# Kernel tuning notes

Measured on AMD Instinct MI355X. Metric: run time of the kernel, lower is better.

## Reference

```python
import jax, jax.numpy as jnp
import numpy as np

B, R, S, H = 4, 64, 512, 768
E = 64            # candidate entities per example
SEG = 128         # seg_emb_dim
NT, NC, NP = 6, 13, 3
REP = 3 * H + 2 * SEG  # rel_rep_size = 2560
NEG = -1e30


def setup_inputs() -> dict:
    key = jax.random.key(0)
    ks = jax.random.split(key, 12)
    hidden_states = jax.random.normal(ks[0], (B, S, H), dtype=jnp.float32)
    rel_pairs = jax.random.randint(ks[1], (B, R, 2), 0, E, dtype=jnp.int64)
    rel_masks = jax.random.randint(ks[2], (B, R, S), 0, 2, dtype=jnp.int32)
    rel_sizes = jax.random.randint(ks[3], (B, R, 2), 0, 30, dtype=jnp.int64)
    ent_span_reps = jax.random.normal(ks[4], (B, E, H), dtype=jnp.float32)
    ent_segs_embs = jax.random.normal(ks[5], (B, E, SEG), dtype=jnp.float32)
    s = 1.0 / np.sqrt(REP)
    W_type = jax.random.uniform(ks[6], (REP, NT), jnp.float32, -s, s)
    b_type = jax.random.uniform(ks[7], (NT,), jnp.float32, -s, s)
    W_cate = jax.random.uniform(ks[8], (REP, NC), jnp.float32, -s, s)
    b_cate = jax.random.uniform(ks[9], (NC,), jnp.float32, -s, s)
    W_pola = jax.random.uniform(ks[10], (REP, NP), jnp.float32, -s, s)
    b_pola = jax.random.uniform(ks[11], (NP,), jnp.float32, -s, s)
    return {"hidden_states": hidden_states, "rel_pairs": rel_pairs,
            "rel_masks": rel_masks, "rel_sizes": rel_sizes,
            "ent_span_reps": ent_span_reps, "ent_segs_embs": ent_segs_embs,
            "W_type": W_type, "b_type": b_type, "W_cate": W_cate,
            "b_cate": b_cate, "W_pola": W_pola, "b_pola": b_pola}


def reference(hidden_states, rel_pairs, rel_masks, rel_sizes,
              ent_span_reps, ent_segs_embs,
              W_type, b_type, W_cate, b_cate, W_pola, b_pola):
    batch, max_rels, _ = rel_pairs.shape
    # batched gather: ent_span_reps[b, rel_pairs[b]] -> [B, R, 2, H] -> [B, R, 2H]
    pair_span = jnp.take_along_axis(
        ent_span_reps[:, :, None, :],
        rel_pairs[:, None, :, :, None].reshape(batch, max_rels * 2, 1, 1), axis=1
    ).reshape(batch, max_rels, -1)
    pair_segs = jnp.take_along_axis(
        ent_segs_embs[:, :, None, :],
        rel_pairs[:, None, :, :, None].reshape(batch, max_rels * 2, 1, 1), axis=1
    ).reshape(batch, max_rels, -1)
    # masked max over seq: scores [B, R, S, H]
    mask_add = (rel_masks == 0).astype(jnp.float32) * NEG          # [B, R, S]
    ctx = jnp.max(hidden_states[:, None, :, :] + mask_add[..., None], axis=2)  # [B, R, H]
    has_ctx = jnp.any(rel_masks != 0, axis=-1)                      # [B, R]
    ctx = jnp.where(has_ctx[..., None], ctx, 0.0)
    features = jnp.concatenate([pair_span, pair_segs, ctx], axis=2)  # [B, R, 2560]
    # dropout is identity at inference
    rel_type_logits = features @ W_type + b_type
    rel_cate_logits = features @ W_cate + b_cate
    rel_pola_logits = features @ W_pola + b_pola
    return (rel_type_logits, rel_cate_logits, rel_pola_logits)
```

## Files before the change

### kernel.cpp

```cpp
#include <hip/hip_runtime.h>
#include <math.h>

#define BB 4
#define RR 64
#define SS 512
#define HH 768
#define EE 64
#define SEGD 128
#define NT 6
#define NC 13
#define NP 3
#define NO (NT + NC + NP)
#define REP 2560
#define NEGV -1e30f

#define HC 8
#define NHB (HH / HC)
#define SCP 4
#define SROWS (SS / SCP)
#define NB1 (BB * NHB * SCP)
#define PART_ELEMS ((size_t)BB * RR * SCP * HH)

__global__ __launch_bounds__(256, 6)
void p1_ctx(const float* __restrict__ hidden,
            const int*   __restrict__ rel_masks,
            float* __restrict__ ws)
{
    const int bid = blockIdx.x;
    const int sc  = bid & 3;
    const int hc  = (bid >> 2) % NHB;
    const int b   = bid / (4 * NHB);
    const int t   = threadIdx.x;
    const int w   = t >> 6;
    const int r   = t & 63;
    const int h0  = hc * HC;
    const int s0  = sc * SROWS;

    __shared__ unsigned char keep[64 * 132];
    __shared__ float part[4 * 64 * 9];

    const int mbase = b * RR * SS + s0;
    for (int k = t; k < 64 * SROWS; k += 256) {
        const int rr = k >> 7;
        const int s  = k & 127;
        keep[rr * 132 + s] = (unsigned char)(rel_masks[(size_t)mbase + rr * SS + s] != 0);
    }
    __syncthreads();

    float a0 = -INFINITY, a1 = -INFINITY, a2 = -INFINITY, a3 = -INFINITY;
    float a4 = -INFINITY, a5 = -INFINITY, a6 = -INFINITY, a7 = -INFINITY;
    const float* hp = hidden + ((size_t)b * SS + s0 + w * 32) * HH + h0;
    const unsigned char* kp = &keep[r * 132 + w * 32];
#pragma unroll 4
    for (int s = 0; s < 32; ++s) {
        const float4 va = *reinterpret_cast<const float4*>(hp + (size_t)s * HH);
        const float4 vb = *reinterpret_cast<const float4*>(hp + (size_t)s * HH + 4);
        const float a = kp[s] ? 0.f : NEGV;
        a0 = fmaxf(a0, va.x + a);
        a1 = fmaxf(a1, va.y + a);
        a2 = fmaxf(a2, va.z + a);
        a3 = fmaxf(a3, va.w + a);
        a4 = fmaxf(a4, vb.x + a);
        a5 = fmaxf(a5, vb.y + a);
        a6 = fmaxf(a6, vb.z + a);
        a7 = fmaxf(a7, vb.w + a);
    }

    float* pp = &part[(w * 64 + r) * 9];
    pp[0] = a0; pp[1] = a1; pp[2] = a2; pp[3] = a3;
    pp[4] = a4; pp[5] = a5; pp[6] = a6; pp[7] = a7;
    __syncthreads();

    if (w == 0) {
        float* wp = ws + (((size_t)(b * RR + r)) * SCP + sc) * HH + h0;
#pragma unroll
        for (int j = 0; j < 8; ++j) {
            float v = part[(0 * 64 + r) * 9 + j];
            v = fmaxf(v, part[(1 * 64 + r) * 9 + j]);
            v = fmaxf(v, part[(2 * 64 + r) * 9 + j]);
            v = fmaxf(v, part[(3 * 64 + r) * 9 + j]);
            wp[j] = v;
        }
    }
}

__global__ __launch_bounds__(256)
void p2_head(const float* __restrict__ ws,
             const int*   __restrict__ rel_pairs,
             const float* __restrict__ span,
             const float* __restrict__ segs,
             const float* __restrict__ Wt, const float* __restrict__ bt,
             const float* __restrict__ Wc, const float* __restrict__ bc,
             const float* __restrict__ Wp, const float* __restrict__ bp,
             float* __restrict__ out)
{
    const int br = blockIdx.x;
    const int b  = br / RR;
    const int t  = threadIdx.x;

    __shared__ float feat[REP];
    __shared__ float red[4][NO];

    const int i0 = rel_pairs[(size_t)br * 2 + 0];
    const int i1 = rel_pairs[(size_t)br * 2 + 1];

    const float* sp0 = span + ((size_t)b * EE + i0) * HH;
    const float* sp1 = span + ((size_t)b * EE + i1) * HH;
    feat[t]            = sp0[t];
    feat[t + 256]      = sp0[t + 256];
    feat[t + 512]      = sp0[t + 512];
    feat[HH + t]       = sp1[t];
    feat[HH + t + 256] = sp1[t + 256];
    feat[HH + t + 512] = sp1[t + 512];
    const float* sg0 = segs + ((size_t)b * EE + i0) * SEGD;
    const float* sg1 = segs + ((size_t)b * EE + i1) * SEGD;
    if (t < SEGD) feat[2 * HH + t] = sg0[t];
    else          feat[2 * HH + SEGD + (t - SEGD)] = sg1[t - SEGD];

    const float* wbase = ws + (size_t)br * SCP * HH;
    float m0 = -INFINITY, m1 = -INFINITY, m2 = -INFINITY;
#pragma unroll
    for (int c = 0; c < SCP; ++c) {
        const float* wp = wbase + (size_t)c * HH;
        m0 = fmaxf(m0, wp[t]);
        m1 = fmaxf(m1, wp[t + 256]);
        m2 = fmaxf(m2, wp[t + 512]);
    }
    if (m0 < -1e29f) m0 = 0.f;
    if (m1 < -1e29f) m1 = 0.f;
    if (m2 < -1e29f) m2 = 0.f;
    const int CTX0 = 2 * HH + 2 * SEGD;
    feat[CTX0 + t]       = m0;
    feat[CTX0 + t + 256] = m1;
    feat[CTX0 + t + 512] = m2;
    __syncthreads();

    float acc[NO];
#pragma unroll
    for (int o = 0; o < NO; ++o) acc[o] = 0.f;
    for (int f = t; f < REP; f += 256) {
        const float fv = feat[f];
        const float* wt = Wt + (size_t)f * NT;
        const float* wc = Wc + (size_t)f * NC;
        const float* wp = Wp + (size_t)f * NP;
#pragma unroll
        for (int o = 0; o < NT; ++o) acc[o]           += fv * wt[o];
#pragma unroll
        for (int o = 0; o < NC; ++o) acc[NT + o]      += fv * wc[o];
#pragma unroll
        for (int o = 0; o < NP; ++o) acc[NT + NC + o] += fv * wp[o];
    }
#pragma unroll
    for (int o = 0; o < NO; ++o) {
#pragma unroll
        for (int off = 32; off > 0; off >>= 1)
            acc[o] += __shfl_down(acc[o], off, 64);
    }
    const int wid  = t >> 6;
    const int lane = t & 63;
    if (lane == 0) {
#pragma unroll
        for (int o = 0; o < NO; ++o) red[wid][o] = acc[o];
    }
    __syncthreads();

    if (t < NO) {
        const float v = red[0][t] + red[1][t] + red[2][t] + red[3][t];
        if (t < NT) {
            out[(size_t)br * NT + t] = v + bt[t];
        } else if (t < NT + NC) {
            const int o = t - NT;
            out[(size_t)BB * RR * NT + (size_t)br * NC + o] = v + bc[o];
        } else {
            const int o = t - NT - NC;
            out[(size_t)BB * RR * (NT + NC) + (size_t)br * NP + o] = v + bp[o];
        }
    }
}

__global__ __launch_bounds__(256)
void rel_cls_fused(const float* __restrict__ hidden,
                   const int*   __restrict__ rel_pairs,
                   const int*   __restrict__ rel_masks,
                   const float* __restrict__ span,
                   const float* __restrict__ segs,
                   const float* __restrict__ Wt, const float* __restrict__ bt,
                   const float* __restrict__ Wc, const float* __restrict__ bc,
                   const float* __restrict__ Wp, const float* __restrict__ bp,
                   float* __restrict__ out)
{
    const int br = blockIdx.x;
    const int b  = br / RR;
    const int t  = threadIdx.x;

    __shared__ float sadd[SS];
    __shared__ float feat[REP];
    __shared__ float red[4][NO];

    const int* mrow = rel_masks + (size_t)br * SS;
    sadd[t]       = mrow[t] ? 0.f : NEGV;
    sadd[t + 256] = mrow[t + 256] ? 0.f : NEGV;

    const int i0 = rel_pairs[(size_t)br * 2 + 0];
    const int i1 = rel_pairs[(size_t)br * 2 + 1];
    const float* sp0 = span + ((size_t)b * EE + i0) * HH;
    const float* sp1 = span + ((size_t)b * EE + i1) * HH;
    feat[t]            = sp0[t];
    feat[t + 256]      = sp0[t + 256];
    feat[t + 512]      = sp0[t + 512];
    feat[HH + t]       = sp1[t];
    feat[HH + t + 256] = sp1[t + 256];
    feat[HH + t + 512] = sp1[t + 512];
    const float* sg0 = segs + ((size_t)b * EE + i0) * SEGD;
    const float* sg1 = segs + ((size_t)b * EE + i1) * SEGD;
    if (t < SEGD) feat[2 * HH + t] = sg0[t];
    else          feat[2 * HH + SEGD + (t - SEGD)] = sg1[t - SEGD];
    __syncthreads();

    float m0 = -INFINITY, m1 = -INFINITY, m2 = -INFINITY;
#pragma unroll 8
    for (int s = 0; s < SS; ++s) {
        const float* hp = hidden + ((size_t)b * SS + s) * HH;
        const float a = sadd[s];
        m0 = fmaxf(m0, hp[t] + a);
        m1 = fmaxf(m1, hp[t + 256] + a);
        m2 = fmaxf(m2, hp[t + 512] + a);
    }
    if (m0 < -1e29f) m0 = 0.f;
    if (m1 < -1e29f) m1 = 0.f;
    if (m2 < -1e29f) m2 = 0.f;
    const int CTX0 = 2 * HH + 2 * SEGD;
    feat[CTX0 + t]       = m0;
    feat[CTX0 + t + 256] = m1;
    feat[CTX0 + t + 512] = m2;
    __syncthreads();

    float acc[NO];
#pragma unroll
    for (int o = 0; o < NO; ++o) acc[o] = 0.f;
    for (int f = t; f < REP; f += 256) {
        const float fv = feat[f];
        const float* wt = Wt + (size_t)f * NT;
        const float* wc = Wc + (size_t)f * NC;
        const float* wp = Wp + (size_t)f * NP;
#pragma unroll
        for (int o = 0; o < NT; ++o) acc[o]           += fv * wt[o];
#pragma unroll
        for (int o = 0; o < NC; ++o) acc[NT + o]      += fv * wc[o];
#pragma unroll
        for (int o = 0; o < NP; ++o) acc[NT + NC + o] += fv * wp[o];
    }
#pragma unroll
    for (int o = 0; o < NO; ++o) {
#pragma unroll
        for (int off = 32; off > 0; off >>= 1)
            acc[o] += __shfl_down(acc[o], off, 64);
    }
    const int wid  = t >> 6;
    const int lane = t & 63;
    if (lane == 0) {
#pragma unroll
        for (int o = 0; o < NO; ++o) red[wid][o] = acc[o];
    }
    __syncthreads();

    if (t < NO) {
        const float v = red[0][t] + red[1][t] + red[2][t] + red[3][t];
        if (t < NT) {
            out[(size_t)br * NT + t] = v + bt[t];
        } else if (t < NT + NC) {
            const int o = t - NT;
            out[(size_t)BB * RR * NT + (size_t)br * NC + o] = v + bc[o];
        } else {
            const int o = t - NT - NC;
            out[(size_t)BB * RR * (NT + NC) + (size_t)br * NP + o] = v + bp[o];
        }
    }
}

extern "C" void kernel_launch(void* const* d_in, const int* in_sizes, int n_in,
                              void* d_out, int out_size, void* d_ws, size_t ws_size,
                              hipStream_t stream) {
    const float* hidden = (const float*)d_in[0];
    const int*   pairs  = (const int*)d_in[1];
    const int*   masks  = (const int*)d_in[2];
    const float* span   = (const float*)d_in[4];
    const float* segs   = (const float*)d_in[5];
    const float* Wt     = (const float*)d_in[6];
    const float* bt     = (const float*)d_in[7];
    const float* Wc     = (const float*)d_in[8];
    const float* bc     = (const float*)d_in[9];
    const float* Wp     = (const float*)d_in[10];
    const float* bp     = (const float*)d_in[11];
    float* out = (float*)d_out;
    float* ws  = (float*)d_ws;

    if (ws_size >= PART_ELEMS * sizeof(float)) {
        hipLaunchKernelGGL(p1_ctx, dim3(NB1), dim3(256), 0, stream,
                           hidden, masks, ws);
        hipLaunchKernelGGL(p2_head, dim3(BB * RR), dim3(256), 0, stream,
                           ws, pairs, span, segs, Wt, bt, Wc, bc, Wp, bp, out);
    } else {
        hipLaunchKernelGGL(rel_cls_fused, dim3(BB * RR), dim3(256), 0, stream,
                           hidden, pairs, masks, span, segs,
                           Wt, bt, Wc, bc, Wp, bp, out);
    }
}
```

Measured before the change: 27.27 us.

## Move gather-feature partial GEMV into first kernel to overlap with masked max

The span/segment gather and their dot products with the head weights now run in extra blocks of the first kernel, alongside the masked-max context blocks. Those blocks write per-relation partial logits (with bias) into the workspace. The second kernel then only reduces the context partials, does the 768-wide context dot product and adds the stored partial logits. This is meant to shorten the serial second kernel and overlap its gather work with the memory-bound max pass. In exchange it needs more workspace and makes the first kernel's grid heavier and uneven, with a larger shared-memory footprint per block that may reduce occupancy.

```diff
diff --git a/kernel.cpp b/kernel.cpp
--- a/kernel.cpp
+++ b/kernel.cpp
@@ -12,6 +12,7 @@
 #define NP 3
 #define NO (NT + NC + NP)
 #define REP 2560
+#define CTX0 (2 * HH + 2 * SEGD)
 #define NEGV -1e30f
 
 #define HC 8
@@ -19,137 +20,187 @@
 #define SCP 4
 #define SROWS (SS / SCP)
 #define NB1 (BB * NHB * SCP)
-#define PART_ELEMS ((size_t)BB * RR * SCP * HH)
+#define NB_G (BB * RR)
+#define CTXP_ELEMS ((size_t)BB * RR * SCP * HH)
+#define SG_OFF CTXP_ELEMS
+#define WS_FLOATS (CTXP_ELEMS + (size_t)BB * RR * NO)
 
 __global__ __launch_bounds__(256, 6)
 void p1_ctx(const float* __restrict__ hidden,
             const int*   __restrict__ rel_masks,
+            const int*   __restrict__ rel_pairs,
+            const float* __restrict__ span,
+            const float* __restrict__ segs,
+            const float* __restrict__ Wt, const float* __restrict__ bt,
+            const float* __restrict__ Wc, const float* __restrict__ bc,
+            const float* __restrict__ Wp, const float* __restrict__ bp,
             float* __restrict__ ws)
 {
     const int bid = blockIdx.x;
-    const int sc  = bid & 3;
-    const int hc  = (bid >> 2) % NHB;
-    const int b   = bid / (4 * NHB);
     const int t   = threadIdx.x;
-    const int w   = t >> 6;
-    const int r   = t & 63;
-    const int h0  = hc * HC;
-    const int s0  = sc * SROWS;
 
     __shared__ unsigned char keep[64 * 132];
     __shared__ float part[4 * 64 * 9];
-
-    const int mbase = b * RR * SS + s0;
-    for (int k = t; k < 64 * SROWS; k += 256) {
-        const int rr = k >> 7;
-        const int s  = k & 127;
-        keep[rr * 132 + s] = (unsigned char)(rel_masks[(size_t)mbase + rr * SS + s] != 0);
-    }
-    __syncthreads();
-
-    float a0 = -INFINITY, a1 = -INFINITY, a2 = -INFINITY, a3 = -INFINITY;
-    float a4 = -INFINITY, a5 = -INFINITY, a6 = -INFINITY, a7 = -INFINITY;
-    const float* hp = hidden + ((size_t)b * SS + s0 + w * 32) * HH + h0;
-    const unsigned char* kp = &keep[r * 132 + w * 32];
+    __shared__ float feat[CTX0];
+    __shared__ float red[4][NO];
+
+    if (bid < NB1) {
+        const int sc  = bid & 3;
+        const int hc  = (bid >> 2) % NHB;
+        const int b   = bid / (4 * NHB);
+        const int w   = t >> 6;
+        const int r   = t & 63;
+        const int h0  = hc * HC;
+        const int s0  = sc * SROWS;
+
+        const int mbase = b * RR * SS + s0;
+        for (int k = t; k < 64 * SROWS; k += 256) {
+            const int rr = k >> 7;
+            const int s  = k & 127;
+            keep[rr * 132 + s] = (unsigned char)(rel_masks[(size_t)mbase + rr * SS + s] != 0);
+        }
+        __syncthreads();
+
+        float a0 = -INFINITY, a1 = -INFINITY, a2 = -INFINITY, a3 = -INFINITY;
+        float a4 = -INFINITY, a5 = -INFINITY, a6 = -INFINITY, a7 = -INFINITY;
+        const float* hp = hidden + ((size_t)b * SS + s0 + w * 32) * HH + h0;
+        const unsigned char* kp = &keep[r * 132 + w * 32];
 #pragma unroll 4
-    for (int s = 0; s < 32; ++s) {
-        const float4 va = *reinterpret_cast<const float4*>(hp + (size_t)s * HH);
-        const float4 vb = *reinterpret_cast<const float4*>(hp + (size_t)s * HH + 4);
-        const float a = kp[s] ? 0.f : NEGV;
-        a0 = fmaxf(a0, va.x + a);
-        a1 = fmaxf(a1, va.y + a);
-        a2 = fmaxf(a2, va.z + a);
-        a3 = fmaxf(a3, va.w + a);
-        a4 = fmaxf(a4, vb.x + a);
-        a5 = fmaxf(a5, vb.y + a);
-        a6 = fmaxf(a6, vb.z + a);
-        a7 = fmaxf(a7, vb.w + a);
-    }
-
-    float* pp = &part[(w * 64 + r) * 9];
-    pp[0] = a0; pp[1] = a1; pp[2] = a2; pp[3] = a3;
-    pp[4] = a4; pp[5] = a5; pp[6] = a6; pp[7] = a7;
-    __syncthreads();
-
-    if (w == 0) {
-        float* wp = ws + (((size_t)(b * RR + r)) * SCP + sc) * HH + h0;
-#pragma unroll
-        for (int j = 0; j < 8; ++j) {
-            float v = part[(0 * 64 + r) * 9 + j];
-            v = fmaxf(v, part[(1 * 64 + r) * 9 + j]);
-            v = fmaxf(v, part[(2 * 64 + r) * 9 + j]);
-            v = fmaxf(v, part[(3 * 64 + r) * 9 + j]);
-            wp[j] = v;
+        for (int s = 0; s < 32; ++s) {
+            const float4 va = *reinterpret_cast<const float4*>(hp + (size_t)s * HH);
+            const float4 vb = *reinterpret_cast<const float4*>(hp + (size_t)s * HH + 4);
+            const float a = kp[s] ? 0.f : NEGV;
+            a0 = fmaxf(a0, va.x + a);
+            a1 = fmaxf(a1, va.y + a);
+            a2 = fmaxf(a2, va.z + a);
+            a3 = fmaxf(a3, va.w + a);
+            a4 = fmaxf(a4, vb.x + a);
+            a5 = fmaxf(a5, vb.y + a);
+            a6 = fmaxf(a6, vb.z + a);
+            a7 = fmaxf(a7, vb.w + a);
+        }
+
+        float* pp = &part[(w * 64 + r) * 9];
+        pp[0] = a0; pp[1] = a1; pp[2] = a2; pp[3] = a3;
+        pp[4] = a4; pp[5] = a5; pp[6] = a6; pp[7] = a7;
+        __syncthreads();
+
+        if (w == 0) {
+            float* wp = ws + (((size_t)(b * RR + r)) * SCP + sc) * HH + h0;
+#pragma unroll
+            for (int j = 0; j < 8; ++j) {
+                float v = part[(0 * 64 + r) * 9 + j];
+                v = fmaxf(v, part[(1 * 64 + r) * 9 + j]);
+                v = fmaxf(v, part[(2 * 64 + r) * 9 + j]);
+                v = fmaxf(v, part[(3 * 64 + r) * 9 + j]);
+                wp[j] = v;
+            }
+        }
+        return;
+    }
+
+    {
+        const int br = bid - NB1;
+        const int b  = br / RR;
+
+        const int i0 = rel_pairs[(size_t)br * 2 + 0];
+        const int i1 = rel_pairs[(size_t)br * 2 + 1];
+
+        const float* sp0 = span + ((size_t)b * EE + i0) * HH;
+        const float* sp1 = span + ((size_t)b * EE + i1) * HH;
+        feat[t]            = sp0[t];
+        feat[t + 256]      = sp0[t + 256];
+        feat[t + 512]      = sp0[t + 512];
+        feat[HH + t]       = sp1[t];
+        feat[HH + t + 256] = sp1[t + 256];
+        feat[HH + t + 512] = sp1[t + 512];
+        const float* sg0 = segs + ((size_t)b * EE + i0) * SEGD;
+        const float* sg1 = segs + ((size_t)b * EE + i1) * SEGD;
+        if (t < SEGD) feat[2 * HH + t] = sg0[t];
+        else          feat[2 * HH + SEGD + (t - SEGD)] = sg1[t - SEGD];
+        __syncthreads();
+
+        float acc[NO];
+#pragma unroll
+        for (int o = 0; o < NO; ++o) acc[o] = 0.f;
+        for (int f = t; f < CTX0; f += 256) {
+            const float fv = feat[f];
+            const float* wt = Wt + (size_t)f * NT;
+            const float* wc = Wc + (size_t)f * NC;
+            const float* wp = Wp + (size_t)f * NP;
+#pragma unroll
+            for (int o = 0; o < NT; ++o) acc[o]           += fv * wt[o];
+#pragma unroll
+            for (int o = 0; o < NC; ++o) acc[NT + o]      += fv * wc[o];
+#pragma unroll
+            for (int o = 0; o < NP; ++o) acc[NT + NC + o] += fv * wp[o];
+        }
+#pragma unroll
+        for (int o = 0; o < NO; ++o) {
+#pragma unroll
+            for (int off = 32; off > 0; off >>= 1)
+                acc[o] += __shfl_down(acc[o], off, 64);
+        }
+        const int wid  = t >> 6;
+        const int lane = t & 63;
+        if (lane == 0) {
+#pragma unroll
+            for (int o = 0; o < NO; ++o) red[wid][o] = acc[o];
+        }
+        __syncthreads();
+
+        if (t < NO) {
+            float v = red[0][t] + red[1][t] + red[2][t] + red[3][t];
+            if (t < NT)           v += bt[t];
+            else if (t < NT + NC) v += bc[t - NT];
+            else                  v += bp[t - NT - NC];
+            ws[SG_OFF + (size_t)br * NO + t] = v;
         }
     }
 }
 
 __global__ __launch_bounds__(256)
 void p2_head(const float* __restrict__ ws,
-             const int*   __restrict__ rel_pairs,
-             const float* __restrict__ span,
-             const float* __restrict__ segs,
-             const float* __restrict__ Wt, const float* __restrict__ bt,
-             const float* __restrict__ Wc, const float* __restrict__ bc,
-             const float* __restrict__ Wp, const float* __restrict__ bp,
+             const float* __restrict__ Wt,
+             const float* __restrict__ Wc,
+             const float* __restrict__ Wp,
              float* __restrict__ out)
 {
     const int br = blockIdx.x;
-    const int b  = br / RR;
     const int t  = threadIdx.x;
 
-    __shared__ float feat[REP];
     __shared__ float red[4][NO];
 
-    const int i0 = rel_pairs[(size_t)br * 2 + 0];
-    const int i1 = rel_pairs[(size_t)br * 2 + 1];
-
-    const float* sp0 = span + ((size_t)b * EE + i0) * HH;
-    const float* sp1 = span + ((size_t)b * EE + i1) * HH;
-    feat[t]            = sp0[t];
-    feat[t + 256]      = sp0[t + 256];
-    feat[t + 512]      = sp0[t + 512];
-    feat[HH + t]       = sp1[t];
-    feat[HH + t + 256] = sp1[t + 256];
-    feat[HH + t + 512] = sp1[t + 512];
-    const float* sg0 = segs + ((size_t)b * EE + i0) * SEGD;
-    const float* sg1 = segs + ((size_t)b * EE + i1) * SEGD;
-    if (t < SEGD) feat[2 * HH + t] = sg0[t];
-    else          feat[2 * HH + SEGD + (t - SEGD)] = sg1[t - SEGD];
-
-    const float* wbase = ws + (size_t)br * SCP * HH;
-    float m0 = -INFINITY, m1 = -INFINITY, m2 = -INFINITY;
-#pragma unroll
-    for (int c = 0; c < SCP; ++c) {
-        const float* wp = wbase + (size_t)c * HH;
-        m0 = fmaxf(m0, wp[t]);
-        m1 = fmaxf(m1, wp[t + 256]);
-        m2 = fmaxf(m2, wp[t + 512]);
-    }
-    if (m0 < -1e29f) m0 = 0.f;
-    if (m1 < -1e29f) m1 = 0.f;
-    if (m2 < -1e29f) m2 = 0.f;
-    const int CTX0 = 2 * HH + 2 * SEGD;
-    feat[CTX0 + t]       = m0;
-    feat[CTX0 + t + 256] = m1;
-    feat[CTX0 + t + 512] = m2;
-    __syncthreads();
+    const float* wb = ws + (size_t)br * SCP * HH;
+    float fv[3];
+#pragma unroll
+    for (int k = 0; k < 3; ++k) {
+        const int col = t + 256 * k;
+        float m = wb[col];
+        m = fmaxf(m, wb[col + HH]);
+        m = fmaxf(m, wb[col + 2 * HH]);
+        m = fmaxf(m, wb[col + 3 * HH]);
+        fv[k] = (m < -1e29f) ? 0.f : m;
+    }
 
     float acc[NO];
 #pragma unroll
     for (int o = 0; o < NO; ++o) acc[o] = 0.f;
-    for (int f = t; f < REP; f += 256) {
-        const float fv = feat[f];
-        const float* wt = Wt + (size_t)f * NT;
-        const float* wc = Wc + (size_t)f * NC;
-        const float* wp = Wp + (size_t)f * NP;
-#pragma unroll
-        for (int o = 0; o < NT; ++o) acc[o]           += fv * wt[o];
-#pragma unroll
-        for (int o = 0; o < NC; ++o) acc[NT + o]      += fv * wc[o];
-#pragma unroll
-        for (int o = 0; o < NP; ++o) acc[NT + NC + o] += fv * wp[o];
-    }
+#pragma unroll
+    for (int k = 0; k < 3; ++k) {
+        const float v  = fv[k];
+        const size_t f = (size_t)(CTX0 + t + 256 * k);
+        const float* wt = Wt + f * NT;
+        const float* wc = Wc + f * NC;
+        const float* wp = Wp + f * NP;
+#pragma unroll
+        for (int o = 0; o < NT; ++o) acc[o]           += v * wt[o];
+#pragma unroll
+        for (int o = 0; o < NC; ++o) acc[NT + o]      += v * wc[o];
+#pragma unroll
+        for (int o = 0; o < NP; ++o) acc[NT + NC + o] += v * wp[o];
+    }
+
 #pragma unroll
     for (int o = 0; o < NO; ++o) {
 #pragma unroll
@@ -165,15 +216,16 @@
     __syncthreads();
 
     if (t < NO) {
-        const float v = red[0][t] + red[1][t] + red[2][t] + red[3][t];
+        const float v = red[0][t] + red[1][t] + red[2][t] + red[3][t]
+                      + ws[SG_OFF + (size_t)br * NO + t];
         if (t < NT) {
-            out[(size_t)br * NT + t] = v + bt[t];
+            out[(size_t)br * NT + t] = v;
         } else if (t < NT + NC) {
             const int o = t - NT;
-            out[(size_t)BB * RR * NT + (size_t)br * NC + o] = v + bc[o];
+            out[(size_t)BB * RR * NT + (size_t)br * NC + o] = v;
         } else {
             const int o = t - NT - NC;
-            out[(size_t)BB * RR * (NT + NC) + (size_t)br * NP + o] = v + bp[o];
+            out[(size_t)BB * RR * (NT + NC) + (size_t)br * NP + o] = v;
         }
     }
 }
@@ -229,7 +281,6 @@
     if (m0 < -1e29f) m0 = 0.f;
     if (m1 < -1e29f) m1 = 0.f;
     if (m2 < -1e29f) m2 = 0.f;
-    const int CTX0 = 2 * HH + 2 * SEGD;
     feat[CTX0 + t]       = m0;
     feat[CTX0 + t + 256] = m1;
     feat[CTX0 + t + 512] = m2;
@@ -295,11 +346,12 @@
     float* out = (float*)d_out;
     float* ws  = (float*)d_ws;
 
-    if (ws_size >= PART_ELEMS * sizeof(float)) {
-        hipLaunchKernelGGL(p1_ctx, dim3(NB1), dim3(256), 0, stream,
-                           hidden, masks, ws);
+    if (ws_size >= WS_FLOATS * sizeof(float)) {
+        hipLaunchKernelGGL(p1_ctx, dim3(NB1 + NB_G), dim3(256), 0, stream,
+                           hidden, masks, pairs, span, segs,
+                           Wt, bt, Wc, bc, Wp, bp, ws);
         hipLaunchKernelGGL(p2_head, dim3(BB * RR), dim3(256), 0, stream,
-                           ws, pairs, span, segs, Wt, bt, Wc, bc, Wp, bp, out);
+                           ws, Wt, Wc, Wp, out);
     } else {
         hipLaunchKernelGGL(rel_cls_fused, dim3(BB * RR), dim3(256), 0, stream,
                            hidden, pairs, masks, span, segs,
```

New measurement: 29.41 us. +7.8%, slower.
